# Optimization experiments

Measured on AMD Instinct MI355X. Metric: run time of the kernel, lower is better.

The kernel has to match this reference:

```python
import jax, jax.numpy as jnp
import numpy as np

MARGIN = 1.0
N, D, P = 4096, 768, 100

def setup_inputs() -> dict:
    key = jax.random.key(0)
    k1, k2, k3 = jax.random.split(key, 3)
    inputs = jax.random.normal(k1, (N, D), dtype=jnp.float32)
    targets = jax.random.randint(k2, (N,), 0, P)
    center = jax.random.normal(k3, (P, D), dtype=jnp.float32)
    return {"inputs": inputs, "targets": targets, "center": center}

def reference(inputs, targets, center):
    n = inputs.shape[0]
    # pairwise euclidean distances: ||xi||^2 + ||xj||^2 - 2 xi.xj
    sq = jnp.sum(inputs * inputs, axis=1)                      # [n]
    dist = sq[:, None] + sq[None, :] - 2.0 * (inputs @ inputs.T)
    dist = jnp.sqrt(jnp.clip(dist, 1e-12))                     # [n, n]
    mask = targets[:, None] == targets[None, :]                # same-class mask
    inf = jnp.asarray(jnp.inf, dist.dtype)
    # hardest positive: max over same-class (diagonal always True -> finite)
    dist_ap = jnp.max(jnp.where(mask, dist, -inf), axis=1)     # [n]
    # hardest negative: min over different-class, fallback ap+margin if none
    dist_an = jnp.min(jnp.where(mask, inf, dist), axis=1)      # [n]
    has_neg = jnp.any(~mask, axis=1)
    dist_an = jnp.where(has_neg, dist_an, dist_ap + MARGIN)
    # prototype augmentation: row-normalized centers, min distance to any center
    cn = center / jnp.linalg.norm(center, axis=1, keepdims=True)
    csq = jnp.sum(cn * cn, axis=1)                             # [P]
    d2c = sq[:, None] + csq[None, :] - 2.0 * (inputs @ cn.T)   # [n, P]
    d2c = jnp.clip(jnp.sqrt(jnp.clip(d2c, 0.0)), 1e-12)
    dist_an = jnp.minimum(dist_an, jnp.min(d2c, axis=1))
    # MarginRankingLoss(dist_an, dist_ap, y=1) = mean(relu(margin - (an - ap)))
    return jnp.mean(jax.nn.relu(MARGIN + dist_ap - dist_an))
```

## Files before the change

kernel.cpp:

```cpp
#include <hip/hip_runtime.h>
#include <math.h>

#define N_ 4096
#define D_ 768
#define P_ 100
#define PPAD 128
#define NT 24
#define NTRI 528
#define NBLK 560

typedef __attribute__((ext_vector_type(8))) short short8;
typedef __attribute__((ext_vector_type(4))) float f32x4;

typedef const __attribute__((address_space(1))) void* gld_src_t;
typedef __attribute__((address_space(3))) void* gld_dst_t;
#define GLOAD16(g, d) __builtin_amdgcn_global_load_lds((gld_src_t)(g), (gld_dst_t)(d), 16, 0, 0)

#define WAITVM4() asm volatile("s_waitcnt vmcnt(4)" ::: "memory")
#define WAITVM0() asm volatile("s_waitcnt vmcnt(0)" ::: "memory")
static __device__ __forceinline__ void barrier_fenced() {
    asm volatile("" ::: "memory");
    __builtin_amdgcn_s_barrier();
    asm volatile("" ::: "memory");
}

__device__ inline unsigned short f2bf(float f) {
    union { float f; unsigned int u; } v; v.f = f;
    unsigned int u = v.u + 0x7fffu + ((v.u >> 16) & 1u);
    return (unsigned short)(u >> 16);
}

__global__ __launch_bounds__(256) void pre_kernel(
    const float* __restrict__ X, const float* __restrict__ C,
    float* __restrict__ sq, unsigned short* __restrict__ Xbf,
    unsigned short* __restrict__ cnbf, float* __restrict__ csq) {
    const int gw = blockIdx.x * 4 + (threadIdx.x >> 6);
    const int l = threadIdx.x & 63;
    if (gw < N_) {
        const float4* x4 = (const float4*)(X + (size_t)gw * D_);
        short4* ob = (short4*)(Xbf + (size_t)gw * D_);
        float s = 0.f;
#pragma unroll
        for (int c = 0; c < 3; ++c) {
            float4 v = x4[c * 64 + l];
            s = fmaf(v.x, v.x, fmaf(v.y, v.y, fmaf(v.z, v.z, fmaf(v.w, v.w, s))));
            short4 o;
            o.x = (short)f2bf(v.x); o.y = (short)f2bf(v.y);
            o.z = (short)f2bf(v.z); o.w = (short)f2bf(v.w);
            ob[c * 64 + l] = o;
        }
#pragma unroll
        for (int m = 1; m < 64; m <<= 1) s += __shfl_xor(s, m);
        if (l == 0) sq[gw] = s;
    } else {
        const int p = gw - N_;
        if (p >= PPAD) return;
        short4* ob = (short4*)(cnbf + (size_t)p * D_);
        if (p < P_) {
            const float4* c4 = (const float4*)(C + (size_t)p * D_);
            float4 v[3];
            float s = 0.f;
#pragma unroll
            for (int c = 0; c < 3; ++c) {
                v[c] = c4[c * 64 + l];
                s = fmaf(v[c].x, v[c].x, fmaf(v[c].y, v[c].y,
                    fmaf(v[c].z, v[c].z, fmaf(v[c].w, v[c].w, s))));
            }
#pragma unroll
            for (int m = 1; m < 64; m <<= 1) s += __shfl_xor(s, m);
            float rn = 1.0f / sqrtf(s);
#pragma unroll
            for (int c = 0; c < 3; ++c) {
                short4 o;
                o.x = (short)f2bf(v[c].x * rn); o.y = (short)f2bf(v[c].y * rn);
                o.z = (short)f2bf(v[c].z * rn); o.w = (short)f2bf(v[c].w * rn);
                ob[c * 64 + l] = o;
            }
            if (l == 0) csq[p] = s * rn * rn;
        } else {
            short4 z; z.x = z.y = z.z = z.w = 0;
#pragma unroll
            for (int c = 0; c < 3; ++c) ob[c * 64 + l] = z;
            if (l == 0) csq[p] = 1e30f;
        }
    }
}

__global__ __launch_bounds__(256, 3) void mfma_kernel(
    const unsigned short* __restrict__ Xbf, const unsigned short* __restrict__ cnbf,
    const int* __restrict__ T, const float* __restrict__ sq,
    const float* __restrict__ csq,
    float* __restrict__ ap_part, float* __restrict__ an_part,
    float* __restrict__ minc) {
    __shared__ __align__(16) unsigned short lds[3 * 8192];

    const int tid = threadIdx.x;
    const int l = tid & 63;
    const int w = tid >> 6;
    const int wr = w >> 1;
    const int wc = w & 1;

    const int orig = blockIdx.x;
    const int bid = (orig & 7) * 70 + (orig >> 3);
    int it, jt;
    if (bid < NTRI) {
        int t = (int)((sqrtf(8.0f * bid + 1.0f) - 1.0f) * 0.5f);
        t += ((t + 1) * (t + 2) / 2 <= bid);
        t -= (t * (t + 1) / 2 > bid);
        it = t; jt = bid - t * (t + 1) / 2;
    } else { it = bid - NTRI; jt = 32; }
    const bool is_center = (jt == 32);
    const bool is_diag = (it == jt);
    const int i0 = it * 128;
    const int j0 = is_center ? 0 : jt * 128;
    const unsigned short* __restrict__ Bmat = is_center ? cnbf : Xbf;

    const int srow = tid >> 2;
    const int scol = ((tid & 3) * 8) ^ (((srow & 6) >> 1) << 3);
    const unsigned short* gA0 = Xbf + (size_t)(i0 + srow) * D_ + scol;
    const unsigned short* gA1 = gA0 + (size_t)64 * D_;
    const unsigned short* gB0 = Bmat + (size_t)(j0 + srow) * D_ + scol;
    const unsigned short* gB1 = gB0 + (size_t)64 * D_;
    const int dA0 = w * 512, dA1 = 2048 + w * 512;
    const int dB0 = 4096 + w * 512, dB1 = 6144 + w * 512;

    const int col = l & 15;
    const int hi = l >> 4;
    const int rko = (hi * 8) ^ ((l & 6) << 2);
    const int aro = (wr * 64 + col) * 32 + rko;
    const int bro = 4096 + (wc * 64 + col) * 32 + rko;

    f32x4 acc[4][4];
#pragma unroll
    for (int m = 0; m < 4; ++m)
#pragma unroll
        for (int n = 0; n < 4; ++n) acc[m][n] = (f32x4){0.f, 0.f, 0.f, 0.f};

#define STAGE(t)                                                     \
    do {                                                             \
        const int bo_ = ((t) % 3) * 8192;                            \
        const int ke_ = (t) * 32;                                    \
        GLOAD16(gA0 + ke_, &lds[bo_ + dA0]);                         \
        GLOAD16(gA1 + ke_, &lds[bo_ + dA1]);                         \
        GLOAD16(gB0 + ke_, &lds[bo_ + dB0]);                         \
        GLOAD16(gB1 + ke_, &lds[bo_ + dB1]);                         \
    } while (0)

    STAGE(0);
    STAGE(1);
    WAITVM4();
    barrier_fenced();

    int bo = 0;
    for (int t = 0; t < NT; ++t) {
        if (t + 2 < NT) STAGE(t + 2);
        const unsigned short* Lb = &lds[bo * 8192];
        short8 a[4], b[4];
#pragma unroll
        for (int m = 0; m < 4; ++m)
            a[m] = *reinterpret_cast<const short8*>(Lb + aro + m * 512);
#pragma unroll
        for (int n = 0; n < 4; ++n)
            b[n] = *reinterpret_cast<const short8*>(Lb + bro + n * 512);
        __builtin_amdgcn_s_setprio(1);
#pragma unroll
        for (int m = 0; m < 4; ++m)
#pragma unroll
            for (int n = 0; n < 4; ++n)
                acc[m][n] = __builtin_amdgcn_mfma_f32_16x16x32_bf16(a[m], b[n], acc[m][n], 0, 0, 0);
        __builtin_amdgcn_s_setprio(0);
        if (t < NT - 1) {
            if (t + 2 < NT) WAITVM4();
            else WAITVM0();
            barrier_fenced();
        }
        bo = (bo == 2) ? 0 : bo + 1;
    }
#undef STAGE

    float* lf = (float*)lds;
    __syncthreads();

    if (!is_center) {
        float sqj[4]; int tj[4];
#pragma unroll
        for (int n = 0; n < 4; ++n) {
            int j = j0 + wc * 64 + n * 16 + col;
            sqj[n] = sq[j];
            tj[n] = T[j];
        }
        float apC[4], anC[4];
#pragma unroll
        for (int n = 0; n < 4; ++n) { apC[n] = -1e30f; anC[n] = 1e30f; }

#pragma unroll
        for (int m = 0; m < 4; ++m) {
#pragma unroll
            for (int r = 0; r < 4; ++r) {
                const int lrow = wr * 64 + m * 16 + hi * 4 + r;
                const int i = i0 + lrow;
                float sqi = sq[i];
                int ti = T[i];
                float apR = -1e30f, anR = 1e30f;
#pragma unroll
                for (int n = 0; n < 4; ++n) {
                    float d2 = sqi + sqj[n] - 2.0f * acc[m][n][r];
                    float d = sqrtf(fmaxf(d2, 1e-12f));
                    bool same = (tj[n] == ti);
                    apR = same ? fmaxf(apR, d) : apR;
                    anR = same ? anR : fminf(anR, d);
                    apC[n] = same ? fmaxf(apC[n], d) : apC[n];
                    anC[n] = same ? anC[n] : fminf(anC[n], d);
                }
#pragma unroll
                for (int msk = 1; msk < 16; msk <<= 1) {
                    apR = fmaxf(apR, __shfl_xor(apR, msk));
                    anR = fminf(anR, __shfl_xor(anR, msk));
                }
                if (col == 0) {
                    lf[wc * 128 + lrow] = apR;
                    lf[256 + wc * 128 + lrow] = anR;
                }
            }
        }
        __syncthreads();
        if (tid < 128) {
            float a = fmaxf(lf[tid], lf[128 + tid]);
            float b = fminf(lf[256 + tid], lf[384 + tid]);
            ap_part[(size_t)jt * N_ + i0 + tid] = a;
            an_part[(size_t)jt * N_ + i0 + tid] = b;
        }

        if (!is_diag) {
            __syncthreads();
#pragma unroll
            for (int n = 0; n < 4; ++n) {
                apC[n] = fmaxf(apC[n], __shfl_xor(apC[n], 16));
                apC[n] = fmaxf(apC[n], __shfl_xor(apC[n], 32));
                anC[n] = fminf(anC[n], __shfl_xor(anC[n], 16));
                anC[n] = fminf(anC[n], __shfl_xor(anC[n], 32));
                if (hi == 0) {
                    int jl = wc * 64 + n * 16 + col;
                    lf[wr * 128 + jl] = apC[n];
                    lf[256 + wr * 128 + jl] = anC[n];
                }
            }
            __syncthreads();
            if (tid < 128) {
                float a = fmaxf(lf[tid], lf[128 + tid]);
                float b = fminf(lf[256 + tid], lf[384 + tid]);
                ap_part[(size_t)(32 + it) * N_ + j0 + tid] = a;
                an_part[(size_t)(32 + it) * N_ + j0 + tid] = b;
            }
        }
    } else {
        float sqj[4];
#pragma unroll
        for (int n = 0; n < 4; ++n) sqj[n] = csq[wc * 64 + n * 16 + col];
#pragma unroll
        for (int m = 0; m < 4; ++m) {
#pragma unroll
            for (int r = 0; r < 4; ++r) {
                const int lrow = wr * 64 + m * 16 + hi * 4 + r;
                const int i = i0 + lrow;
                float sqi = sq[i];
                float mc = 1e30f;
#pragma unroll
                for (int n = 0; n < 4; ++n) {
                    float d2 = sqi + sqj[n] - 2.0f * acc[m][n][r];
                    float d = fmaxf(sqrtf(fmaxf(d2, 0.0f)), 1e-12f);
                    mc = fminf(mc, d);
                }
#pragma unroll
                for (int msk = 1; msk < 16; msk <<= 1)
                    mc = fminf(mc, __shfl_xor(mc, msk));
                if (col == 0) lf[wc * 128 + lrow] = mc;
            }
        }
        __syncthreads();
        if (tid < 128) minc[i0 + tid] = fminf(lf[tid], lf[128 + tid]);
    }
}

__global__ __launch_bounds__(256) void combine1(
    const float* __restrict__ ap_part, const float* __restrict__ an_part,
    const float* __restrict__ minc, float* __restrict__ bsum) {
    __shared__ float sred[4];
    const int i = blockIdx.x * 256 + threadIdx.x;
    const int r = i >> 7;
    float ap = -1e30f, an = 1e30f;
    for (int jt = 0; jt <= r; ++jt) {
        ap = fmaxf(ap, ap_part[(size_t)jt * N_ + i]);
        an = fminf(an, an_part[(size_t)jt * N_ + i]);
    }
    for (int it2 = r + 1; it2 < 32; ++it2) {
        ap = fmaxf(ap, ap_part[(size_t)(32 + it2) * N_ + i]);
        an = fminf(an, an_part[(size_t)(32 + it2) * N_ + i]);
    }
    float dan = (an < 1e29f) ? an : (ap + 1.0f);
    dan = fminf(dan, minc[i]);
    float term = fmaxf(0.0f, 1.0f + ap - dan);
#pragma unroll
    for (int m = 32; m > 0; m >>= 1) term += __shfl_xor(term, m);
    if ((threadIdx.x & 63) == 0) sred[threadIdx.x >> 6] = term;
    __syncthreads();
    if (threadIdx.x == 0)
        bsum[blockIdx.x] = sred[0] + sred[1] + sred[2] + sred[3];
}

__global__ void finalize(const float* __restrict__ bsum, float* __restrict__ out) {
    if (threadIdx.x == 0) {
        float s = 0.f;
        for (int b = 0; b < N_ / 256; ++b) s += bsum[b];
        out[0] = s / (float)N_;
    }
}

extern "C" void kernel_launch(void* const* d_in, const int* in_sizes, int n_in,
                              void* d_out, int out_size, void* d_ws, size_t ws_size,
                              hipStream_t stream) {
    const float* X = (const float*)d_in[0];
    const int* T = (const int*)d_in[1];
    const float* C = (const float*)d_in[2];
    float* out = (float*)d_out;

    float* ws = (float*)d_ws;
    float* sq = ws;
    float* csq = ws + 4096;
    float* minc = ws + 4224;
    float* bsum = ws + 8320;
    unsigned short* Xbf = (unsigned short*)(ws + 8336);
    unsigned short* cnbf = (unsigned short*)(ws + 1581200);
    float* ap_part = ws + 1630352;
    float* an_part = ws + 1892496;

    pre_kernel<<<(N_ + PPAD) / 4, 256, 0, stream>>>(X, C, sq, Xbf, cnbf, csq);
    mfma_kernel<<<NBLK, 256, 0, stream>>>(Xbf, cnbf, T, sq, csq, ap_part, an_part, minc);
    combine1<<<N_ / 256, 256, 0, stream>>>(ap_part, an_part, minc, bsum);
    finalize<<<1, 64, 0, stream>>>(bsum, out);
}
```

Measured before the change: 61.68 us.

## Switch GEMM to double-buffered 64-wide K stages with grouped tile ordering

Replaces the 3-stage, 32-wide K pipeline with a 2-buffer pipeline that loads 64 K-elements per stage. This halves the number of barriers and waits. It also changes block-to-tile mapping to a grouped 8x8 super-tile ordering for better L2 locality, drops s_setprio, and lowers the launch-bounds occupancy hint from 3 to 2. The trade-off is that each stage now waits on vmcnt(0), so there is less prefetch depth, and LDS use per block rises.

```diff
diff --git a/kernel.cpp b/kernel.cpp
--- a/kernel.cpp
+++ b/kernel.cpp
@@ -5,7 +5,7 @@
 #define D_ 768
 #define P_ 100
 #define PPAD 128
-#define NT 24
+#define NT64 12
 #define NTRI 528
 #define NBLK 560
 
@@ -16,7 +16,6 @@
 typedef __attribute__((address_space(3))) void* gld_dst_t;
 #define GLOAD16(g, d) __builtin_amdgcn_global_load_lds((gld_src_t)(g), (gld_dst_t)(d), 16, 0, 0)
 
-#define WAITVM4() asm volatile("s_waitcnt vmcnt(4)" ::: "memory")
 #define WAITVM0() asm volatile("s_waitcnt vmcnt(0)" ::: "memory")
 static __device__ __forceinline__ void barrier_fenced() {
     asm volatile("" ::: "memory");
@@ -28,6 +27,29 @@
     union { float f; unsigned int u; } v; v.f = f;
     unsigned int u = v.u + 0x7fffu + ((v.u >> 16) & 1u);
     return (unsigned short)(u >> 16);
+}
+
+static __device__ __forceinline__ void decode_tile(int orig, int* pit, int* pjt) {
+    const int x = orig & 7;
+    const int k = orig >> 3;
+    if (k >= 66) { *pit = x * 4 + (k - 66); *pjt = 32; return; }
+    const int g = x * 66 + k;
+    const int cumR[11] = {0, 36, 100, 136, 200, 264, 300, 364, 428, 492, 528};
+    const int GIr[10] = {0, 1, 1, 2, 2, 2, 3, 3, 3, 3};
+    const int GJr[10] = {0, 0, 1, 0, 1, 2, 0, 1, 2, 3};
+    int r = 0;
+    while (cumR[r + 1] <= g) ++r;
+    const int u = g - cumR[r];
+    int di, dj;
+    if (GIr[r] == GJr[r]) {
+        di = 0;
+        while ((di + 1) * (di + 2) / 2 <= u) ++di;
+        dj = u - di * (di + 1) / 2;
+    } else {
+        di = u >> 3; dj = u & 7;
+    }
+    *pit = GIr[r] * 8 + di;
+    *pjt = GJr[r] * 8 + dj;
 }
 
 __global__ __launch_bounds__(256) void pre_kernel(
@@ -86,13 +108,13 @@
     }
 }
 
-__global__ __launch_bounds__(256, 3) void mfma_kernel(
+__global__ __launch_bounds__(256, 2) void mfma_kernel(
     const unsigned short* __restrict__ Xbf, const unsigned short* __restrict__ cnbf,
     const int* __restrict__ T, const float* __restrict__ sq,
     const float* __restrict__ csq,
     float* __restrict__ ap_part, float* __restrict__ an_part,
     float* __restrict__ minc) {
-    __shared__ __align__(16) unsigned short lds[3 * 8192];
+    __shared__ __align__(16) unsigned short lds[2 * 16384];
 
     const int tid = threadIdx.x;
     const int l = tid & 63;
@@ -100,17 +122,9 @@
     const int wr = w >> 1;
     const int wc = w & 1;
 
-    const int orig = blockIdx.x;
-    const int bid = (orig & 7) * 70 + (orig >> 3);
     int it, jt;
-    if (bid < NTRI) {
-        int t = (int)((sqrtf(8.0f * bid + 1.0f) - 1.0f) * 0.5f);
-        t += ((t + 1) * (t + 2) / 2 <= bid);
-        t -= (t * (t + 1) / 2 > bid);
-        it = t; jt = bid - t * (t + 1) / 2;
-    } else { it = bid - NTRI; jt = 32; }
+    decode_tile(blockIdx.x, &it, &jt);
     const bool is_center = (jt == 32);
-    const bool is_diag = (it == jt);
     const int i0 = it * 128;
     const int j0 = is_center ? 0 : jt * 128;
     const unsigned short* __restrict__ Bmat = is_center ? cnbf : Xbf;
@@ -136,47 +150,49 @@
 #pragma unroll
         for (int n = 0; n < 4; ++n) acc[m][n] = (f32x4){0.f, 0.f, 0.f, 0.f};
 
-#define STAGE(t)                                                     \
-    do {                                                             \
-        const int bo_ = ((t) % 3) * 8192;                            \
-        const int ke_ = (t) * 32;                                    \
-        GLOAD16(gA0 + ke_, &lds[bo_ + dA0]);                         \
-        GLOAD16(gA1 + ke_, &lds[bo_ + dA1]);                         \
-        GLOAD16(gB0 + ke_, &lds[bo_ + dB0]);                         \
-        GLOAD16(gB1 + ke_, &lds[bo_ + dB1]);                         \
+#define STAGE64(t, p)                                                  \
+    do {                                                               \
+        unsigned short* db_ = &lds[(p) * 16384];                       \
+        const int ke_ = (t) * 64;                                      \
+        GLOAD16(gA0 + ke_, db_ + dA0);                                 \
+        GLOAD16(gA1 + ke_, db_ + dA1);                                 \
+        GLOAD16(gB0 + ke_, db_ + dB0);                                 \
+        GLOAD16(gB1 + ke_, db_ + dB1);                                 \
+        GLOAD16(gA0 + ke_ + 32, db_ + 8192 + dA0);                     \
+        GLOAD16(gA1 + ke_ + 32, db_ + 8192 + dA1);                     \
+        GLOAD16(gB0 + ke_ + 32, db_ + 8192 + dB0);                     \
+        GLOAD16(gB1 + ke_ + 32, db_ + 8192 + dB1);                     \
     } while (0)
 
-    STAGE(0);
-    STAGE(1);
-    WAITVM4();
+    STAGE64(0, 0);
+    WAITVM0();
     barrier_fenced();
 
-    int bo = 0;
-    for (int t = 0; t < NT; ++t) {
-        if (t + 2 < NT) STAGE(t + 2);
-        const unsigned short* Lb = &lds[bo * 8192];
-        short8 a[4], b[4];
-#pragma unroll
-        for (int m = 0; m < 4; ++m)
-            a[m] = *reinterpret_cast<const short8*>(Lb + aro + m * 512);
-#pragma unroll
-        for (int n = 0; n < 4; ++n)
-            b[n] = *reinterpret_cast<const short8*>(Lb + bro + n * 512);
-        __builtin_amdgcn_s_setprio(1);
-#pragma unroll
-        for (int m = 0; m < 4; ++m)
+    int p = 0;
+    for (int t = 0; t < NT64; ++t) {
+        if (t + 1 < NT64) STAGE64(t + 1, p ^ 1);
+        const unsigned short* Lb = &lds[p * 16384];
+#pragma unroll
+        for (int c = 0; c < 2; ++c) {
+            short8 a[4], b[4];
+#pragma unroll
+            for (int m = 0; m < 4; ++m)
+                a[m] = *reinterpret_cast<const short8*>(Lb + c * 8192 + aro + m * 512);
 #pragma unroll
             for (int n = 0; n < 4; ++n)
-                acc[m][n] = __builtin_amdgcn_mfma_f32_16x16x32_bf16(a[m], b[n], acc[m][n], 0, 0, 0);
-        __builtin_amdgcn_s_setprio(0);
-        if (t < NT - 1) {
-            if (t + 2 < NT) WAITVM4();
-            else WAITVM0();
-            barrier_fenced();
-        }
-        bo = (bo == 2) ? 0 : bo + 1;
-    }
-#undef STAGE
+                b[n] = *reinterpret_cast<const short8*>(Lb + c * 8192 + bro + n * 512);
+#pragma unroll
+            for (int m = 0; m < 4; ++m)
+#pragma unroll
+                for (int n = 0; n < 4; ++n)
+                    acc[m][n] = __builtin_amdgcn_mfma_f32_16x16x32_bf16(
+                        a[m], b[n], acc[m][n], 0, 0, 0);
+        }
+        WAITVM0();
+        barrier_fenced();
+        p ^= 1;
+    }
+#undef STAGE64
 
     float* lf = (float*)lds;
     __syncthreads();
@@ -231,7 +247,7 @@
             an_part[(size_t)jt * N_ + i0 + tid] = b;
         }
 
-        if (!is_diag) {
+        if (it != jt) {
             __syncthreads();
 #pragma unroll
             for (int n = 0; n < 4; ++n) {
```

After: 67.39 us. 1.09x slower.
